# Kernel optimization log

Measured on AMD Instinct MI355X. Metric: run time of the kernel, lower is better.

## Reference

```python
import jax, jax.numpy as jnp
import numpy as np


def setup_inputs() -> dict:
    key = jax.random.key(0)
    k1, k2, k3 = jax.random.split(key, 3)
    N, C, H, W, K = 64, 128, 64, 64, 64
    x = jax.random.normal(k1, (N, C, H, W), dtype=jnp.float32)
    conv_w = jax.random.normal(k2, (K, C), dtype=jnp.float32) * 0.05
    centroids = jax.random.uniform(k3, (K, C), dtype=jnp.float32)
    return {"x": x, "conv_w": conv_w, "centroids": centroids}


def reference(x, conv_w, centroids):
    # x: [N, C, H, W]; conv_w: [K, C] (1x1 conv, no bias); centroids: [K, C]
    n, c = x.shape[:2]
    x_flat = x.reshape(n, c, -1)                      # [N, C, S]
    # 1x1 conv == per-pixel linear map, then softmax over clusters
    logits = jnp.einsum('kc,ncs->nks', conv_w, x_flat)  # [N, K, S]
    a = jax.nn.softmax(logits, axis=1)                  # softmax over K
    # VLAD: sum_s a[n,k,s] * (x[n,:,s] - centroid[k])
    #     = (a @ x^T) - (sum_s a) * centroid   -- two batched GEMMs, no [N,K,C,S] blowup
    vlad = jnp.einsum('nks,ncs->nkc', a, x_flat) - a.sum(axis=-1)[..., None] * centroids[None]
    # intra-normalization (L2 per cluster), flatten, global L2
    vlad = vlad / jnp.linalg.norm(vlad, axis=2, keepdims=True)
    vlad = vlad.reshape(n, -1)
    vlad = vlad / jnp.linalg.norm(vlad, axis=1, keepdims=True)
    return vlad
```

## Files before the change

kernel.cpp:

```cpp
#include <hip/hip_runtime.h>


#define Nn 64
#define Cc 128
#define Ss 4096
#define Kk 64
#define TS 64
#define CH 8
#define SB (TS*CH)
#define Pp 8

typedef __attribute__((ext_vector_type(8))) short bf16x8;
typedef __attribute__((ext_vector_type(4))) float f32x4;

__device__ __forceinline__ unsigned f2bf(float f) {
  unsigned u = __float_as_uint(f);
  u = (u + 0x7FFFu + ((u >> 16) & 1u)) >> 16;
  return u;
}

#define XSC_STR 136
#define XCS_STR 72
#define AKS_STR 72

__launch_bounds__(256, 2)
__global__ void netvlad_main(const float* __restrict__ x,
                             const float* __restrict__ w,
                             float* __restrict__ vlad,
                             float* __restrict__ asum,
                             int use_atomic)
{
  __shared__ __align__(16) unsigned short x_sc[TS][XSC_STR];
  __shared__ __align__(16) unsigned short x_cs[Cc][XCS_STR];
  __shared__ __align__(16) unsigned short a_ks[Kk][AKS_STR];

  const int t   = threadIdx.x;
  const int wv  = t >> 6;
  const int l15 = t & 15;
  const int l4  = (t >> 4) & 3;
  const int n   = blockIdx.y;
  const int sb  = blockIdx.x;
  const size_t xbase = (size_t)n * Cc * Ss;

  bf16x8 wfrag[4][4];
#pragma unroll
  for (int mt = 0; mt < 4; ++mt) {
#pragma unroll
    for (int q = 0; q < 4; ++q) {
      const float* wp = w + (16*mt + l15) * Cc + 32*q + 8*l4;
      float4 a = *(const float4*)wp;
      float4 b = *(const float4*)(wp + 4);
      bf16x8 f;
      f[0] = (short)f2bf(a.x); f[1] = (short)f2bf(a.y);
      f[2] = (short)f2bf(a.z); f[3] = (short)f2bf(a.w);
      f[4] = (short)f2bf(b.x); f[5] = (short)f2bf(b.y);
      f[6] = (short)f2bf(b.z); f[7] = (short)f2bf(b.w);
      wfrag[mt][q] = f;
    }
  }

  f32x4 acc3[4][2];
#pragma unroll
  for (int mt = 0; mt < 4; ++mt)
#pragma unroll
    for (int tc = 0; tc < 2; ++tc) acc3[mt][tc] = (f32x4){0.f,0.f,0.f,0.f};
  float asum_reg[4][4];
#pragma unroll
  for (int mt = 0; mt < 4; ++mt)
#pragma unroll
    for (int r = 0; r < 4; ++r) asum_reg[mt][r] = 0.f;

  const int s4 = 4 * l15;
  const int cb = t >> 4;
  float4 v[8];
  {
    const float* px = x + xbase + (size_t)cb * Ss + sb * SB + s4;
#pragma unroll
    for (int it = 0; it < 8; ++it)
      v[it] = *(const float4*)(px + (size_t)(16 * it) * Ss);
  }

  for (int ch = 0; ch < CH; ++ch) {
    const int s0 = sb * SB + ch * TS;

#pragma unroll
    for (int it = 0; it < 8; ++it) {
      float4 vv = v[it];
      unsigned p0 = f2bf(vv.x) | (f2bf(vv.y) << 16);
      unsigned p1 = f2bf(vv.z) | (f2bf(vv.w) << 16);
      *(int2*)&x_cs[cb + 16*it][s4] = make_int2((int)p0, (int)p1);
    }
    if (ch + 1 < CH) {
      const float* px = x + xbase + (size_t)cb * Ss + s0 + TS + s4;
#pragma unroll
      for (int it = 0; it < 8; ++it)
        v[it] = *(const float4*)(px + (size_t)(16 * it) * Ss);
    }
    __syncthreads();

    {
      const int srow = 16*wv + l15;
#pragma unroll
      for (int j = 0; j < 4; ++j) {
        const int c8 = 32*j + 8*l4;
        unsigned short h[8];
#pragma unroll
        for (int i = 0; i < 8; ++i) {
          const int i2 = (i + 2*l4) & 7;
          h[i2] = x_cs[c8 + i2][srow];
        }
        unsigned p0 = (unsigned)h[0] | ((unsigned)h[1] << 16);
        unsigned p1 = (unsigned)h[2] | ((unsigned)h[3] << 16);
        unsigned p2 = (unsigned)h[4] | ((unsigned)h[5] << 16);
        unsigned p3 = (unsigned)h[6] | ((unsigned)h[7] << 16);
        *(int4*)&x_sc[srow][c8] = make_int4((int)p0, (int)p1, (int)p2, (int)p3);
      }
    }

    f32x4 acc1[4];
#pragma unroll
    for (int mt = 0; mt < 4; ++mt) acc1[mt] = (f32x4){0.f,0.f,0.f,0.f};
#pragma unroll
    for (int q = 0; q < 4; ++q) {
      bf16x8 bfr = *(bf16x8*)&x_sc[16*wv + l15][32*q + 8*l4];
#pragma unroll
      for (int mt = 0; mt < 4; ++mt)
        acc1[mt] = __builtin_amdgcn_mfma_f32_16x16x32_bf16(wfrag[mt][q], bfr, acc1[mt], 0, 0, 0);
    }

    float e[4][4];
    float cs = 0.f;
#pragma unroll
    for (int mt = 0; mt < 4; ++mt)
#pragma unroll
      for (int r = 0; r < 4; ++r) {
        float ev = __expf(acc1[mt][r]);
        e[mt][r] = ev;
        cs += ev;
      }
    cs += __shfl_xor(cs, 16, 64);
    cs += __shfl_xor(cs, 32, 64);
    const float inv = 1.0f / cs;
#pragma unroll
    for (int mt = 0; mt < 4; ++mt)
#pragma unroll
      for (int r = 0; r < 4; ++r) {
        float an = e[mt][r] * inv;
        asum_reg[mt][r] += an;
        a_ks[16*mt + 4*l4 + r][16*wv + l15] = (unsigned short)f2bf(an);
      }
    __syncthreads();

#pragma unroll
    for (int q2 = 0; q2 < 2; ++q2) {
      bf16x8 afr[4];
#pragma unroll
      for (int mt = 0; mt < 4; ++mt)
        afr[mt] = *(bf16x8*)&a_ks[16*mt + l15][32*q2 + 8*l4];
#pragma unroll
      for (int tc = 0; tc < 2; ++tc) {
        bf16x8 bfr = *(bf16x8*)&x_cs[32*wv + 16*tc + l15][32*q2 + 8*l4];
#pragma unroll
        for (int mt = 0; mt < 4; ++mt)
          acc3[mt][tc] = __builtin_amdgcn_mfma_f32_16x16x32_bf16(afr[mt], bfr, acc3[mt][tc], 0, 0, 0);
      }
    }
    __syncthreads();
  }

  float* asml = (float*)a_ks;
#pragma unroll
  for (int mt = 0; mt < 4; ++mt) {
#pragma unroll
    for (int r = 0; r < 4; ++r) {
      float vv = asum_reg[mt][r];
      vv += __shfl_xor(vv, 1, 64);
      vv += __shfl_xor(vv, 2, 64);
      vv += __shfl_xor(vv, 4, 64);
      vv += __shfl_xor(vv, 8, 64);
      if (l15 == 0) asml[wv * Kk + 16*mt + 4*l4 + r] = vv;
    }
  }
  __syncthreads();
  if (t < Kk) {
    float s = asml[t] + asml[Kk + t] + asml[2*Kk + t] + asml[3*Kk + t];
    if (use_atomic) atomicAdd(&asum[n * Kk + t], s);
    else            asum[((size_t)sb * Nn + n) * Kk + t] = s;
  }

  if (use_atomic) {
#pragma unroll
    for (int mt = 0; mt < 4; ++mt)
#pragma unroll
      for (int tc = 0; tc < 2; ++tc)
#pragma unroll
        for (int r = 0; r < 4; ++r) {
          const int k = 16*mt + 4*l4 + r;
          const int c = 32*wv + 16*tc + l15;
          atomicAdd(&vlad[((size_t)n * Kk + k) * Cc + c], acc3[mt][tc][r]);
        }
  } else {
    float* vp = vlad + ((size_t)sb * Nn + n) * (Kk * Cc);
#pragma unroll
    for (int mt = 0; mt < 4; ++mt)
#pragma unroll
      for (int tc = 0; tc < 2; ++tc)
#pragma unroll
        for (int r = 0; r < 4; ++r) {
          const int k = 16*mt + 4*l4 + r;
          const int c = 32*wv + 16*tc + l15;
          vp[k * Cc + c] = acc3[mt][tc][r];
        }
  }
}

__global__ void netvlad_epilogue(const float* __restrict__ vlad,
                                 const float* __restrict__ asum,
                                 const float* __restrict__ cent,
                                 float* __restrict__ out,
                                 int nparts)
{
  const int n  = blockIdx.x;
  const int k  = 16*blockIdx.y + (threadIdx.x >> 4);
  const int cq = threadIdx.x & 15;

  float ak = 0.f;
  float4 x0 = make_float4(0.f, 0.f, 0.f, 0.f);
  float4 x1 = make_float4(0.f, 0.f, 0.f, 0.f);
  for (int p = 0; p < nparts; ++p) {
    ak += asum[((size_t)p * Nn + n) * Kk + k];
    const float* vp = vlad + (((size_t)p * Nn + n) * Kk + k) * Cc + 8*cq;
    float4 a0 = *(const float4*)vp;
    float4 a1 = *(const float4*)(vp + 4);
    x0.x += a0.x; x0.y += a0.y; x0.z += a0.z; x0.w += a0.w;
    x1.x += a1.x; x1.y += a1.y; x1.z += a1.z; x1.w += a1.w;
  }

  const size_t cbse = (size_t)k * Cc + 8*cq;
  float4 c0 = *(const float4*)(cent + cbse);
  float4 c1 = *(const float4*)(cent + cbse + 4);
  float4 r0, r1;
  r0.x = x0.x - ak*c0.x; r0.y = x0.y - ak*c0.y; r0.z = x0.z - ak*c0.z; r0.w = x0.w - ak*c0.w;
  r1.x = x1.x - ak*c1.x; r1.y = x1.y - ak*c1.y; r1.z = x1.z - ak*c1.z; r1.w = x1.w - ak*c1.w;
  float ss = r0.x*r0.x + r0.y*r0.y + r0.z*r0.z + r0.w*r0.w
           + r1.x*r1.x + r1.y*r1.y + r1.z*r1.z + r1.w*r1.w;
  ss += __shfl_xor(ss, 1, 64);
  ss += __shfl_xor(ss, 2, 64);
  ss += __shfl_xor(ss, 4, 64);
  ss += __shfl_xor(ss, 8, 64);
  const float rn = rsqrtf(ss) * 0.125f;
  r0.x *= rn; r0.y *= rn; r0.z *= rn; r0.w *= rn;
  r1.x *= rn; r1.y *= rn; r1.z *= rn; r1.w *= rn;
  float* op = out + (size_t)n * (Kk * Cc) + (size_t)k * Cc + 8*cq;
  *(float4*)op = r0;
  *(float4*)(op + 4) = r1;
}

extern "C" void kernel_launch(void* const* d_in, const int* in_sizes, int n_in,
                              void* d_out, int out_size, void* d_ws, size_t ws_size,
                              hipStream_t stream)
{
  const float* x    = (const float*)d_in[0];
  const float* w    = (const float*)d_in[1];
  const float* cent = (const float*)d_in[2];
  float* out = (float*)d_out;

  const size_t vlad_elems_p = (size_t)Pp * Nn * Kk * Cc;
  const size_t asum_elems_p = (size_t)Pp * Nn * Kk;
  const size_t need = (vlad_elems_p + asum_elems_p) * sizeof(float);

  if (ws_size >= need) {
    float* vlad_part = (float*)d_ws;
    float* asum_part = vlad_part + vlad_elems_p;
    netvlad_main<<<dim3(Pp, Nn), 256, 0, stream>>>(x, w, vlad_part, asum_part, 0);
    netvlad_epilogue<<<dim3(Nn, 4), 256, 0, stream>>>(vlad_part, asum_part, cent, out, Pp);
  } else {
    float* vlad = (float*)d_ws;
    float* asum = vlad + (size_t)Nn * Kk * Cc;
    const size_t zbytes = ((size_t)Nn * Kk * Cc + (size_t)Nn * Kk) * sizeof(float);
    hipMemsetAsync(d_ws, 0, zbytes, stream);
    netvlad_main<<<dim3(Pp, Nn), 256, 0, stream>>>(x, w, vlad, asum, 1);
    netvlad_epilogue<<<dim3(Nn, 4), 256, 0, stream>>>(vlad, asum, cent, out, 1);
  }
}
```

Baseline: 210.6 us.

## Double-buffer x tile in LDS, drop transpose staging and trailing barrier

Gives the bf16 x tile in shared memory two buffers that alternate between iterations, so the barrier at the end of each chunk iteration can be removed. The separate x_sc transpose buffer is dropped; each wave now gathers its GEMM operand fragments from x_cs straight into registers. __syncthreads is replaced by a hand-written wait-on-LDS plus s_barrier. The launch bound rises to 3 blocks per CU, and the chunks per block are halved (CH 8→4, Pp 8→16) to create more blocks, which means more partial sums for the later reduction. The risks are extra register pressure from holding the fragments in registers and the cost of the larger partial-sum reduction.

```diff
diff --git a/kernel.cpp b/kernel.cpp
--- a/kernel.cpp
+++ b/kernel.cpp
@@ -6,9 +6,9 @@
 #define Ss 4096
 #define Kk 64
 #define TS 64
-#define CH 8
+#define CH 4
 #define SB (TS*CH)
-#define Pp 8
+#define Pp 16
 
 typedef __attribute__((ext_vector_type(8))) short bf16x8;
 typedef __attribute__((ext_vector_type(4))) float f32x4;
@@ -19,19 +19,21 @@
   return u;
 }
 
-#define XSC_STR 136
+__device__ __forceinline__ void bar_lds() {
+  asm volatile("s_waitcnt lgkmcnt(0)\n\ts_barrier" ::: "memory");
+}
+
 #define XCS_STR 72
 #define AKS_STR 72
 
-__launch_bounds__(256, 2)
+__launch_bounds__(256, 3)
 __global__ void netvlad_main(const float* __restrict__ x,
                              const float* __restrict__ w,
                              float* __restrict__ vlad,
                              float* __restrict__ asum,
                              int use_atomic)
 {
-  __shared__ __align__(16) unsigned short x_sc[TS][XSC_STR];
-  __shared__ __align__(16) unsigned short x_cs[Cc][XCS_STR];
+  __shared__ __align__(16) unsigned short x_cs[2][Cc][XCS_STR];
   __shared__ __align__(16) unsigned short a_ks[Kk][AKS_STR];
 
   const int t   = threadIdx.x;
@@ -72,49 +74,44 @@
 
   const int s4 = 4 * l15;
   const int cb = t >> 4;
+  const float* px0 = x + xbase + (size_t)cb * Ss + sb * SB + s4;
   float4 v[8];
-  {
-    const float* px = x + xbase + (size_t)cb * Ss + sb * SB + s4;
-#pragma unroll
-    for (int it = 0; it < 8; ++it)
-      v[it] = *(const float4*)(px + (size_t)(16 * it) * Ss);
-  }
+#pragma unroll
+  for (int it = 0; it < 8; ++it)
+    v[it] = *(const float4*)(px0 + (size_t)(16 * it) * Ss);
 
   for (int ch = 0; ch < CH; ++ch) {
-    const int s0 = sb * SB + ch * TS;
+    const int buf = ch & 1;
 
 #pragma unroll
     for (int it = 0; it < 8; ++it) {
       float4 vv = v[it];
       unsigned p0 = f2bf(vv.x) | (f2bf(vv.y) << 16);
       unsigned p1 = f2bf(vv.z) | (f2bf(vv.w) << 16);
-      *(int2*)&x_cs[cb + 16*it][s4] = make_int2((int)p0, (int)p1);
+      *(int2*)&x_cs[buf][cb + 16*it][s4] = make_int2((int)p0, (int)p1);
     }
     if (ch + 1 < CH) {
-      const float* px = x + xbase + (size_t)cb * Ss + s0 + TS + s4;
+      const float* px = px0 + (ch + 1) * TS;
 #pragma unroll
       for (int it = 0; it < 8; ++it)
         v[it] = *(const float4*)(px + (size_t)(16 * it) * Ss);
     }
-    __syncthreads();
-
-    {
-      const int srow = 16*wv + l15;
-#pragma unroll
-      for (int j = 0; j < 4; ++j) {
-        const int c8 = 32*j + 8*l4;
-        unsigned short h[8];
-#pragma unroll
-        for (int i = 0; i < 8; ++i) {
-          const int i2 = (i + 2*l4) & 7;
-          h[i2] = x_cs[c8 + i2][srow];
-        }
-        unsigned p0 = (unsigned)h[0] | ((unsigned)h[1] << 16);
-        unsigned p1 = (unsigned)h[2] | ((unsigned)h[3] << 16);
-        unsigned p2 = (unsigned)h[4] | ((unsigned)h[5] << 16);
-        unsigned p3 = (unsigned)h[6] | ((unsigned)h[7] << 16);
-        *(int4*)&x_sc[srow][c8] = make_int4((int)p0, (int)p1, (int)p2, (int)p3);
-      }
+    bar_lds();
+
+    bf16x8 bfr[4];
+#pragma unroll
+    for (int j = 0; j < 4; ++j) {
+      const int c8 = 32*j + 8*l4;
+      unsigned short h[8];
+#pragma unroll
+      for (int i = 0; i < 8; ++i) {
+        const int i2 = (i + 2*l4) & 7;
+        h[i2] = x_cs[buf][c8 + i2][16*wv + l15];
+      }
+      bf16x8 f;
+#pragma unroll
+      for (int i = 0; i < 8; ++i) f[i] = (short)h[i];
+      bfr[j] = f;
     }
 
     f32x4 acc1[4];
@@ -122,10 +119,9 @@
     for (int mt = 0; mt < 4; ++mt) acc1[mt] = (f32x4){0.f,0.f,0.f,0.f};
 #pragma unroll
     for (int q = 0; q < 4; ++q) {
-      bf16x8 bfr = *(bf16x8*)&x_sc[16*wv + l15][32*q + 8*l4];
 #pragma unroll
       for (int mt = 0; mt < 4; ++mt)
-        acc1[mt] = __builtin_amdgcn_mfma_f32_16x16x32_bf16(wfrag[mt][q], bfr, acc1[mt], 0, 0, 0);
+        acc1[mt] = __builtin_amdgcn_mfma_f32_16x16x32_bf16(wfrag[mt][q], bfr[q], acc1[mt], 0, 0, 0);
     }
 
     float e[4][4];
@@ -149,7 +145,7 @@
         asum_reg[mt][r] += an;
         a_ks[16*mt + 4*l4 + r][16*wv + l15] = (unsigned short)f2bf(an);
       }
-    __syncthreads();
+    bar_lds();
 
 #pragma unroll
     for (int q2 = 0; q2 < 2; ++q2) {
@@ -159,15 +155,15 @@
         afr[mt] = *(bf16x8*)&a_ks[16*mt + l15][32*q2 + 8*l4];
 #pragma unroll
       for (int tc = 0; tc < 2; ++tc) {
-        bf16x8 bfr = *(bf16x8*)&x_cs[32*wv + 16*tc + l15][32*q2 + 8*l4];
+        bf16x8 bfx = *(bf16x8*)&x_cs[buf][32*wv + 16*tc + l15][32*q2 + 8*l4];
 #pragma unroll
         for (int mt = 0; mt < 4; ++mt)
-          acc3[mt][tc] = __builtin_amdgcn_mfma_f32_16x16x32_bf16(afr[mt], bfr, acc3[mt][tc], 0, 0, 0);
-      }
-    }
-    __syncthreads();
-  }
-
+          acc3[mt][tc] = __builtin_amdgcn_mfma_f32_16x16x32_bf16(afr[mt], bfx, acc3[mt][tc], 0, 0, 0);
+      }
+    }
+  }
+
+  __syncthreads();
   float* asml = (float*)a_ks;
 #pragma unroll
   for (int mt = 0; mt < 4; ++mt) {
```

Result: slower. 253.6 us (+20.4%).
